# Optimization experiments

Hardware: AMD Instinct MI355X
Metric: run time of the kernel (lower is better)

## Reference

```python
import jax, jax.numpy as jnp
import numpy as np
import math

B, H, N, D = 4, 8, 2048, 64


def setup_inputs() -> dict:
    key = jax.random.key(0)
    kq, kk, kv = jax.random.split(key, 3)
    q = jax.random.normal(kq, (B, H, N, D), dtype=jnp.float32)
    k = jax.random.normal(kk, (B, H, N, D), dtype=jnp.float32)
    v = jax.random.normal(kv, (B, H, N, D), dtype=jnp.float32)
    return {"q": q, "k": k, "v": v}


def reference(q, k, v):
    # global_attention_Sub: expanded squared L2 distance ||q_i - k_j||^2
    # = qq_i - 2 q_i.k_j + kk_j, then softmax(-dist/sqrt(D)) @ v.
    scale = math.sqrt(q.shape[-1])
    inner = -2.0 * jnp.einsum('bhnd,bhmd->bhnm', q, k)          # [B,H,N,N]
    qq = jnp.sum(q * q, axis=-1, keepdims=True)                  # [B,H,N,1]
    kk = jnp.sum(k * k, axis=-1, keepdims=True)                  # [B,H,N,1]
    diff_sq = qq + inner + jnp.swapaxes(kk, -1, -2)              # [B,H,N,N]
    attn = jax.nn.softmax(-diff_sq / scale, axis=-1)
    x = jnp.einsum('bhnm,bhmd->bhnd', attn, v)                   # [B,H,N,D]
    return jnp.transpose(x, (0, 2, 1, 3))                        # [B,N,H,D]
```

## Files before the change

kernel.cpp:

```cpp
#include <hip/hip_runtime.h>

typedef __bf16 bf16x8 __attribute__((ext_vector_type(8)));
typedef float floatx4 __attribute__((ext_vector_type(4)));
typedef float floatx16 __attribute__((ext_vector_type(16)));
typedef unsigned int uintx4 __attribute__((ext_vector_type(4)));

constexpr int Bc = 4, Hc = 8, Nc = 2048, Dc = 64;
constexpr int BQ = 128;
constexpr int WQ = 32;
constexpr int TK = 64;
constexpr int NT = Nc / TK;
constexpr float LOG2E = 1.44269504088896340736f;

constexpr size_t KSW_OFF = 0;
constexpr size_t VSW_OFF = (size_t)32 * NT * 8192;
constexpr size_t KKN_OFF = VSW_OFF * 2;

typedef __attribute__((address_space(1))) const unsigned int gu32;
typedef __attribute__((address_space(3))) unsigned int lu32;
__device__ __forceinline__ void dma16(const void* g, void* l) {
    __builtin_amdgcn_global_load_lds((gu32*)g, (lu32*)l, 16, 0, 0);
}

__device__ __forceinline__ unsigned pk2(float lo, float hi) {
    unsigned short a = __builtin_bit_cast(unsigned short, (__bf16)lo);
    unsigned short b = __builtin_bit_cast(unsigned short, (__bf16)hi);
    return (unsigned)a | ((unsigned)b << 16);
}

__global__ __launch_bounds__(256) void prep_kernel(
    const float* __restrict__ Kg, const float* __restrict__ Vg, char* __restrict__ ws)
{
    __shared__ float sT[64 * 68];
    const int tid = threadIdx.x;
    const int jt = blockIdx.x, bh = blockIdx.y;

    __bf16* Ksw = (__bf16*)(ws + KSW_OFF) + ((size_t)bh * NT + jt) * 4096;
    __bf16* Vsw = (__bf16*)(ws + VSW_OFF) + ((size_t)bh * NT + jt) * 4096;
    float*  kkn = (float*)(ws + KKN_OFF) + (size_t)bh * Nc + jt * 64;
    const size_t tb = ((size_t)bh * Nc + jt * 64) * Dc;

#pragma unroll
    for (int cc = 0; cc < 2; ++cc) {
        const int g   = tid + cc * 256;
        const int key = g >> 3, kcx = g & 7;
        const int kc  = kcx ^ (key & 7);
        const float* src = Kg + tb + key * 64 + kc * 8;
        float4 a = *(const float4*)src;
        float4 b = *(const float4*)(src + 4);
        float ss = a.x*a.x + a.y*a.y + a.z*a.z + a.w*a.w
                 + b.x*b.x + b.y*b.y + b.z*b.z + b.w*b.w;
        ss += __shfl_xor(ss, 1);
        ss += __shfl_xor(ss, 2);
        ss += __shfl_xor(ss, 4);
        if (kcx == 0) {
            const int k5 = key & 31, kt = key >> 5;
            const int rlo = k5 & 3, hh = (k5 >> 2) & 1, rhi = k5 >> 3;
            kkn[kt * 32 + hh * 16 + rhi * 4 + rlo] = -(ss * 0.125f * LOG2E);
        }
        bf16x8 c8;
        c8[0]=(__bf16)a.x; c8[1]=(__bf16)a.y; c8[2]=(__bf16)a.z; c8[3]=(__bf16)a.w;
        c8[4]=(__bf16)b.x; c8[5]=(__bf16)b.y; c8[6]=(__bf16)b.z; c8[7]=(__bf16)b.w;
        *(bf16x8*)(Ksw + g * 8) = c8;
    }
    {
        const int js = tid >> 2, dc = (tid & 3) * 16;
        const float* vr = Vg + tb + js * 64 + dc;
        float* dst = &sT[js * 68 + dc];
        *(float4*)dst       = *(const float4*)vr;
        *(float4*)(dst + 4) = *(const float4*)(vr + 4);
        *(float4*)(dst + 8) = *(const float4*)(vr + 8);
        *(float4*)(dst + 12)= *(const float4*)(vr + 12);
    }
    __syncthreads();
#pragma unroll
    for (int cc = 0; cc < 2; ++cc) {
        const int g = tid + cc * 256;
        const int d = g >> 3, kcx = g & 7;
        const int kc = kcx ^ (d & 7);
        bf16x8 c8;
#pragma unroll
        for (int e = 0; e < 8; ++e) {
            const int ee = (e + kcx) & 7;
            c8[ee] = (__bf16)sT[(kc * 8 + ee) * 68 + d];
        }
        *(bf16x8*)(Vsw + g * 8) = c8;
    }
}

__global__ __launch_bounds__(256, 4) void attn_kernel(
    const float* __restrict__ Qg, const char* __restrict__ ws, float* __restrict__ Og)
{
    __shared__ __align__(16) __bf16 sK[2][4096];
    __shared__ __align__(16) __bf16 sV[2][4096];
    __shared__ __align__(16) float  sl[BQ];

    const int tid  = threadIdx.x;
    const int wave = tid >> 6;
    const int lane = tid & 63;
    const int r31  = lane & 31;
    const int hi   = lane >> 5;

    const int qt = blockIdx.x;
    const int bh = blockIdx.y;

    const char* Kimg = ws + KSW_OFF + (size_t)bh * NT * 8192;
    const char* Vimg = ws + VSW_OFF + (size_t)bh * NT * 8192;
    const float* kkp = (const float*)(ws + KKN_OFF) + (size_t)bh * Nc;

    const float qscale = 0.25f * LOG2E;
    const int i0 = qt * BQ + wave * WQ;

    bf16x8 qf[4];
    {
        const float* qrow = Qg + ((size_t)bh * Nc + i0 + r31) * Dc + hi * 8;
#pragma unroll
        for (int ks = 0; ks < 4; ++ks) {
            float4 a = *(const float4*)(qrow + ks * 16);
            float4 b = *(const float4*)(qrow + ks * 16 + 4);
            bf16x8 f;
            f[0] = (__bf16)(a.x * qscale); f[1] = (__bf16)(a.y * qscale);
            f[2] = (__bf16)(a.z * qscale); f[3] = (__bf16)(a.w * qscale);
            f[4] = (__bf16)(b.x * qscale); f[5] = (__bf16)(b.y * qscale);
            f[6] = (__bf16)(b.z * qscale); f[7] = (__bf16)(b.w * qscale);
            qf[ks] = f;
        }
    }

    int off4[4];
#pragma unroll
    for (int ks = 0; ks < 4; ++ks)
        off4[ks] = r31 * 128 + (((ks * 2 + hi) ^ (r31 & 7)) << 4);

    floatx16 oacc[2];
#pragma unroll
    for (int dt = 0; dt < 2; ++dt)
#pragma unroll
        for (int e = 0; e < 16; ++e) oacc[dt][e] = 0.f;
    float lpr = 0.f;

    auto stage = [&](int jt2, int nb) {
        const char* ki = Kimg + (size_t)jt2 * 8192;
        const char* vi = Vimg + (size_t)jt2 * 8192;
        const int off = tid * 16;
        dma16(ki + off,        (char*)&sK[nb][0] + off);
        dma16(ki + off + 4096, (char*)&sK[nb][0] + off + 4096);
        dma16(vi + off,        (char*)&sV[nb][0] + off);
        dma16(vi + off + 4096, (char*)&sV[nb][0] + off + 4096);
    };

    stage(0, 0);

    for (int jt = 0; jt < NT; ++jt) {
        const int b = jt & 1;
        __syncthreads();
        if (jt + 1 < NT) stage(jt + 1, b ^ 1);

        floatx16 st[2];
        const float* kkb = kkp + jt * 64 + hi * 16;
#pragma unroll
        for (int kt = 0; kt < 2; ++kt) {
#pragma unroll
            for (int gi = 0; gi < 4; ++gi) {
                floatx4 kv = *(const floatx4*)(kkb + kt * 32 + gi * 4);
                st[kt][gi * 4 + 0] = kv[0]; st[kt][gi * 4 + 1] = kv[1];
                st[kt][gi * 4 + 2] = kv[2]; st[kt][gi * 4 + 3] = kv[3];
            }
        }

        const char* kb = (const char*)&sK[b][0];
#pragma unroll
        for (int kt = 0; kt < 2; ++kt)
#pragma unroll
            for (int ks = 0; ks < 4; ++ks) {
                bf16x8 kf = *(const bf16x8*)(kb + kt * 4096 + off4[ks]);
                st[kt] = __builtin_amdgcn_mfma_f32_32x32x16_bf16(kf, qf[ks], st[kt], 0, 0, 0);
            }

        const char* vb = (const char*)&sV[b][0];
#pragma unroll
        for (int kt = 0; kt < 2; ++kt) {
            float p[16];
#pragma unroll
            for (int r = 0; r < 16; ++r) {
                p[r] = __builtin_amdgcn_exp2f(st[kt][r]);
                lpr += p[r];
            }
            unsigned w[4][2];
#pragma unroll
            for (int g = 0; g < 4; ++g) {
                w[g][0] = pk2(p[4 * g + 0], p[4 * g + 1]);
                w[g][1] = pk2(p[4 * g + 2], p[4 * g + 3]);
            }
#pragma unroll
            for (int sub = 0; sub < 2; ++sub) {
                unsigned a0 = w[2 * sub][0],     a1 = w[2 * sub][1];
                unsigned b0 = w[2 * sub + 1][0], b1 = w[2 * sub + 1][1];
                asm("v_permlane32_swap_b32 %0, %1" : "+v"(a0), "+v"(b0));
                asm("v_permlane32_swap_b32 %0, %1" : "+v"(a1), "+v"(b1));
                uintx4 u; u[0] = a0; u[1] = a1; u[2] = b0; u[3] = b1;
                bf16x8 pa = __builtin_bit_cast(bf16x8, u);
                const int ks = kt * 2 + sub;
#pragma unroll
                for (int dt = 0; dt < 2; ++dt) {
                    bf16x8 vf = *(const bf16x8*)(vb + dt * 4096 + off4[ks]);
                    oacc[dt] = __builtin_amdgcn_mfma_f32_32x32x16_bf16(pa, vf, oacc[dt], 0, 0, 0);
                }
            }
        }
    }

    {
        float l = lpr + __shfl_xor(lpr, 32);
        if (!hi) sl[wave * 32 + r31] = l;
    }
    const int b_ = bh >> 3, hh = bh & 7;
#pragma unroll
    for (int g = 0; g < 4; ++g) {
        floatx4 lf = *(const floatx4*)&sl[wave * 32 + 8 * g + 4 * hi];
#pragma unroll
        for (int rlo = 0; rlo < 4; ++rlo) {
            const float inv = 1.f / lf[rlo];
            const int i = i0 + 8 * g + 4 * hi + rlo;
            float* orow = Og + (((size_t)b_ * Nc + i) * Hc + hh) * Dc + r31;
            const int r = 4 * g + rlo;
            orow[0]  = oacc[0][r] * inv;
            orow[32] = oacc[1][r] * inv;
        }
    }
}

extern "C" void kernel_launch(void* const* d_in, const int* in_sizes, int n_in,
                              void* d_out, int out_size, void* d_ws, size_t ws_size,
                              hipStream_t stream) {
    const float* q = (const float*)d_in[0];
    const float* k = (const float*)d_in[1];
    const float* v = (const float*)d_in[2];
    float* out = (float*)d_out;
    char* ws = (char*)d_ws;
    prep_kernel<<<dim3(NT, Bc * Hc), 256, 0, stream>>>(k, v, ws);
    attn_kernel<<<dim3(Nc / BQ, Bc * Hc), 256, 0, stream>>>(q, ws, out);
}
```

Measured before the change: 155.9 us.

## Split key tiles across two wave groups per block with LDS reduction

Doubles the block to 512 threads and splits the key/value tiles between two groups of four waves, each processing alternate tiles of a doubled staging buffer. At the end, partial outputs and row sums are exchanged and reduced through shared memory. This halves the number of loop iterations and barriers per block and increases in-flight work. In exchange it needs more LDS per block (possibly lower block occupancy) and adds an extra reduction epilogue.

```diff
diff --git a/kernel.cpp b/kernel.cpp
--- a/kernel.cpp
+++ b/kernel.cpp
@@ -10,11 +10,18 @@
 constexpr int WQ = 32;
 constexpr int TK = 64;
 constexpr int NT = Nc / TK;
+constexpr int NT2 = NT / 2;
 constexpr float LOG2E = 1.44269504088896340736f;
 
 constexpr size_t KSW_OFF = 0;
 constexpr size_t VSW_OFF = (size_t)32 * NT * 8192;
 constexpr size_t KKN_OFF = VSW_OFF * 2;
+
+constexpr int SK_OFF = 0;
+constexpr int SV_OFF = 32768;
+constexpr int SL_OFF = 65536;
+constexpr int EXCH_OFF = 0;
+constexpr int SMEM_BYTES = 65536 + 1024;
 
 typedef __attribute__((address_space(1))) const unsigned int gu32;
 typedef __attribute__((address_space(3))) unsigned int lu32;
@@ -88,15 +95,15 @@
     }
 }
 
-__global__ __launch_bounds__(256, 4) void attn_kernel(
+__global__ __launch_bounds__(512, 4) void attn_kernel(
     const float* __restrict__ Qg, const char* __restrict__ ws, float* __restrict__ Og)
 {
-    __shared__ __align__(16) __bf16 sK[2][4096];
-    __shared__ __align__(16) __bf16 sV[2][4096];
-    __shared__ __align__(16) float  sl[BQ];
+    __shared__ __align__(16) char smem[SMEM_BYTES];
 
     const int tid  = threadIdx.x;
     const int wave = tid >> 6;
+    const int grp  = wave >> 2;
+    const int sw   = wave & 3;
     const int lane = tid & 63;
     const int r31  = lane & 31;
     const int hi   = lane >> 5;
@@ -109,7 +116,7 @@
     const float* kkp = (const float*)(ws + KKN_OFF) + (size_t)bh * Nc;
 
     const float qscale = 0.25f * LOG2E;
-    const int i0 = qt * BQ + wave * WQ;
+    const int i0 = qt * BQ + sw * WQ;
 
     bf16x8 qf[4];
     {
@@ -139,22 +146,25 @@
         for (int e = 0; e < 16; ++e) oacc[dt][e] = 0.f;
     float lpr = 0.f;
 
-    auto stage = [&](int jt2, int nb) {
-        const char* ki = Kimg + (size_t)jt2 * 8192;
-        const char* vi = Vimg + (size_t)jt2 * 8192;
+    auto stage = [&](int t2, int nb) {
+        const size_t tb = (size_t)(2 * t2) * 8192;
         const int off = tid * 16;
-        dma16(ki + off,        (char*)&sK[nb][0] + off);
-        dma16(ki + off + 4096, (char*)&sK[nb][0] + off + 4096);
-        dma16(vi + off,        (char*)&sV[nb][0] + off);
-        dma16(vi + off + 4096, (char*)&sV[nb][0] + off + 4096);
+        dma16(Kimg + tb + off,        smem + SK_OFF + nb * 8192 + off);
+        dma16(Kimg + tb + 8192 + off, smem + SK_OFF + 16384 + nb * 8192 + off);
+        dma16(Vimg + tb + off,        smem + SV_OFF + nb * 8192 + off);
+        dma16(Vimg + tb + 8192 + off, smem + SV_OFF + 16384 + nb * 8192 + off);
     };
 
     stage(0, 0);
 
-    for (int jt = 0; jt < NT; ++jt) {
-        const int b = jt & 1;
+    for (int t = 0; t < NT2; ++t) {
+        const int b = t & 1;
         __syncthreads();
-        if (jt + 1 < NT) stage(jt + 1, b ^ 1);
+        if (t + 1 < NT2) stage(t + 1, b ^ 1);
+
+        const int jt = 2 * t + grp;
+        const char* kb = smem + SK_OFF + grp * 16384 + b * 8192;
+        const char* vb = smem + SV_OFF + grp * 16384 + b * 8192;
 
         floatx16 st[2];
         const float* kkb = kkp + jt * 64 + hi * 16;
@@ -168,7 +178,6 @@
             }
         }
 
-        const char* kb = (const char*)&sK[b][0];
 #pragma unroll
         for (int kt = 0; kt < 2; ++kt)
 #pragma unroll
@@ -177,7 +186,6 @@
                 st[kt] = __builtin_amdgcn_mfma_f32_32x32x16_bf16(kf, qf[ks], st[kt], 0, 0, 0);
             }
 
-        const char* vb = (const char*)&sV[b][0];
 #pragma unroll
         for (int kt = 0; kt < 2; ++kt) {
             float p[16];
@@ -212,20 +220,45 @@
 
     {
         float l = lpr + __shfl_xor(lpr, 32);
-        if (!hi) sl[wave * 32 + r31] = l;
-    }
+        if (!hi) *(float*)(smem + SL_OFF + (grp * 128 + sw * 32 + r31) * 4) = l;
+    }
+    __syncthreads();
+
+    {
+        char* slot = smem + EXCH_OFF + wave * 4096;
+        if (grp == 0) {
+#pragma unroll
+            for (int r = 0; r < 16; ++r)
+                *(float*)(slot + r * 256 + lane * 4) = oacc[1][r];
+        } else {
+#pragma unroll
+            for (int r = 0; r < 16; ++r)
+                *(float*)(slot + r * 256 + lane * 4) = oacc[0][r];
+        }
+    }
+    __syncthreads();
+
+    floatx16 osum;
+    if (grp == 0) osum = oacc[0]; else osum = oacc[1];
+    {
+        const char* slot = smem + EXCH_OFF + (wave ^ 4) * 4096;
+#pragma unroll
+        for (int r = 0; r < 16; ++r)
+            osum[r] += *(const float*)(slot + r * 256 + lane * 4);
+    }
+
+    const float* slp = (const float*)(smem + SL_OFF);
     const int b_ = bh >> 3, hh = bh & 7;
 #pragma unroll
     for (int g = 0; g < 4; ++g) {
-        floatx4 lf = *(const floatx4*)&sl[wave * 32 + 8 * g + 4 * hi];
+        floatx4 la = *(const floatx4*)(slp + sw * 32 + 8 * g + 4 * hi);
+        floatx4 lb = *(const floatx4*)(slp + 128 + sw * 32 + 8 * g + 4 * hi);
 #pragma unroll
         for (int rlo = 0; rlo < 4; ++rlo) {
-            const float inv = 1.f / lf[rlo];
+            const float inv = 1.f / (la[rlo] + lb[rlo]);
             const int i = i0 + 8 * g + 4 * hi + rlo;
-            float* orow = Og + (((size_t)b_ * Nc + i) * Hc + hh) * Dc + r31;
-            const int r = 4 * g + rlo;
-            orow[0]  = oacc[0][r] * inv;
-            orow[32] = oacc[1][r] * inv;
+            float* orow = Og + (((size_t)b_ * Nc + i) * Hc + hh) * Dc + grp * 32 + r31;
+            orow[0] = osum[4 * g + rlo] * inv;
         }
     }
 }
@@ -239,5 +272,5 @@
     float* out = (float*)d_out;
     char* ws = (char*)d_ws;
     prep_kernel<<<dim3(NT, Bc * Hc), 256, 0, stream>>>(k, v, ws);
-    attn_kernel<<<dim3(Nc / BQ, Bc * Hc), 256, 0, stream>>>(q, ws, out);
-}
+    attn_kernel<<<dim3(Nc / BQ, Bc * Hc), 512, 0, stream>>>(q, ws, out);
+}
```

Result: faster. 140.1 us (-10.1%).
